# Optimization experiments

Hardware: AMD Instinct MI355X
Metric: run time of the kernel (lower is better)

Reference implementation:

```python
import jax, jax.numpy as jnp
import numpy as np

# SamplesLoss('sinkhorn', p=2, blur=0.05, scaling=0.9), tensorized backend,
# debiased Sinkhorn divergence with log-domain softmin and eps annealing.
P = 2
BLUR = 0.05
SCALING = 0.9
# geomloss uses the data-dependent max diameter; we fix a conservative constant
# (randn clouds in 64-D have pairwise distances ~ sqrt(2*64) ~ 11.3) so the
# epsilon schedule length is static / jit-friendly.
DIAMETER = 16.0


def _eps_schedule():
    e = np.arange(P * np.log(DIAMETER), P * np.log(BLUR), P * np.log(SCALING))
    return np.concatenate([np.exp(e), [BLUR ** P]]).astype(np.float32)  # ~56 steps


def _sqdist(x, y):
    # x: [N,D], y: [M,D] -> [N,M] squared euclidean distances
    return (jnp.sum(x * x, -1)[:, None] + jnp.sum(y * y, -1)[None, :]
            - 2.0 * x @ y.T)


def _softmin(eps, C, h):
    # h: [M] = log-weights + potential/eps ; C: [N,M]
    return -eps * jax.nn.logsumexp(h[None, :] - C / eps, axis=1)


def _sinkhorn_divergence(xb, yb, eps_list):
    # xb: [N,D], yb: [M,D]; uniform weights a=1/N, b=1/M
    N, M = xb.shape[0], yb.shape[0]
    C_xy = 0.5 * _sqdist(xb, yb)   # p=2 cost: |x-y|^2 / 2
    C_yx = C_xy.T
    C_xx = 0.5 * _sqdist(xb, xb)
    C_yy = 0.5 * _sqdist(yb, yb)
    a_log = jnp.full((N,), -float(np.log(N)), C_xy.dtype)
    b_log = jnp.full((M,), -float(np.log(M)), C_xy.dtype)

    # geomloss runs the annealing loop with autograd off; grads come only from
    # the final extrapolation step.
    Cxy_d, Cyx_d, Cxx_d, Cyy_d = map(jax.lax.stop_gradient,
                                     (C_xy, C_yx, C_xx, C_yy))

    eps0 = float(eps_list[0])
    f_ba = _softmin(eps0, Cxy_d, b_log)
    g_ab = _softmin(eps0, Cyx_d, a_log)
    f_aa = _softmin(eps0, Cxx_d, a_log)
    g_bb = _softmin(eps0, Cyy_d, b_log)

    def step(carry, eps):
        f_ba, g_ab, f_aa, g_bb = carry
        ft = _softmin(eps, Cxy_d, b_log + g_ab / eps)
        gt = _softmin(eps, Cyx_d, a_log + f_ba / eps)
        fa = _softmin(eps, Cxx_d, a_log + f_aa / eps)
        gb = _softmin(eps, Cyy_d, b_log + g_bb / eps)
        return (0.5 * (f_ba + ft), 0.5 * (g_ab + gt),
                0.5 * (f_aa + fa), 0.5 * (g_bb + gb)), None

    (f_ba, g_ab, f_aa, g_bb), _ = jax.lax.scan(
        step, (f_ba, g_ab, f_aa, g_bb), jnp.asarray(eps_list))

    # last extrapolation at eps = blur^p, no averaging, with gradients
    eps = float(eps_list[-1])
    f_ba_f = _softmin(eps, C_xy, b_log + g_ab / eps)
    g_ab_f = _softmin(eps, C_yx, a_log + f_ba / eps)
    f_aa_f = _softmin(eps, C_xx, a_log + f_aa / eps)
    g_bb_f = _softmin(eps, C_yy, b_log + g_bb / eps)

    a = jnp.exp(a_log)
    b = jnp.exp(b_log)
    return jnp.dot(a, f_ba_f - f_aa_f) + jnp.dot(b, g_ab_f - g_bb_f)


def setup_inputs() -> dict:
    key = jax.random.key(0)
    k1, k2 = jax.random.split(key)
    x = jax.random.normal(k1, (4, 64, 64, 64), dtype=jnp.float32)
    y = jax.random.normal(k2, (4, 64, 64, 64), dtype=jnp.float32)
    return {"x": x, "y": y}


def reference(x, y):
    B, C, H, W = x.shape
    xf = x.reshape(B, C, H * W).transpose(0, 2, 1)  # [B, N, C]
    yf = y.reshape(B, C, H * W).transpose(0, 2, 1)
    eps_list = _eps_schedule()
    losses = jax.vmap(lambda xb, yb: _sinkhorn_divergence(xb, yb, eps_list))(xf, yf)
    return jnp.sum(losses) / B
```

## Files before the change

kernel.cpp:

```cpp
#include <hip/hip_runtime.h>
#include <cmath>

#define NPTS 4096
#define LOG2E_F 1.4426950408889634f
#define LN2_F   0.6931471805599453f
#define BLOG_F  -8.31776616671934f

#if __has_builtin(__builtin_amdgcn_exp2f)
#define EXP2F(x) __builtin_amdgcn_exp2f(x)
#else
#define EXP2F(x) exp2f(x)
#endif
#if __has_builtin(__builtin_amdgcn_logf)
#define LOG2F(x) __builtin_amdgcn_logf(x)
#else
#define LOG2F(x) log2f(x)
#endif

typedef __attribute__((ext_vector_type(8))) short s16x8;
typedef __attribute__((ext_vector_type(4))) float f32x4;

#define GAS __attribute__((address_space(1)))
#define LAS __attribute__((address_space(3)))

__device__ __forceinline__ ushort bf16h(float f) {
    uint u = __float_as_uint(f);
    return (ushort)((u + 0x7fffu + ((u >> 16) & 1u)) >> 16);
}
__device__ __forceinline__ float bf16tof(ushort h) {
    return __uint_as_float(((uint)h) << 16);
}

__global__ __launch_bounds__(256) void norms_kernel(const float* __restrict__ x,
                                                    const float* __restrict__ y,
                                                    float* __restrict__ norms,
                                                    float* __restrict__ aux0) {
    int flat = blockIdx.x * 256 + threadIdx.x;
    int which = flat >> 14;
    int rem = flat & 16383;
    int b = rem >> 12;
    int i = rem & 4095;
    const float* p = (which ? y : x) + (size_t)b * 64 * NPTS + i;
    float s = 0.f;
#pragma unroll
    for (int c = 0; c < 64; ++c) {
        float v = p[(size_t)c * NPTS];
        s += v * v;
    }
    s *= 0.5f;
    norms[flat] = s;
    aux0[(size_t)((which ? 1 : 0) * 4 + b) * NPTS + i] = -s;
    aux0[(size_t)((which ? 3 : 2) * 4 + b) * NPTS + i] = -s;
}

__global__ __launch_bounds__(256) void split_kernel(const float* __restrict__ x,
                                                    const float* __restrict__ y,
                                                    ushort* __restrict__ split) {
    int flat = blockIdx.x * 256 + threadIdx.x;
    int n = flat & 4095;
    int g = (flat >> 12) & 7;
    int b = (flat >> 15) & 3;
    int which = flat >> 17;
    const float* src = (which ? y : x) + (size_t)b * 64 * NPTS + (size_t)g * 8 * NPTS + n;
    size_t base = ((size_t)(which * 4 + b) * 32 + (n >> 7)) * 2048 + (n & 127);
    ushort hh[8], ll[8];
#pragma unroll
    for (int e = 0; e < 8; ++e) {
        float v = src[(size_t)e * NPTS];
        hh[e] = bf16h(v);
        ll[e] = bf16h(v - bf16tof(hh[e]));
    }
    uint4 hw, lw;
    hw.x = (uint)hh[0] | ((uint)hh[1] << 16);
    hw.y = (uint)hh[2] | ((uint)hh[3] << 16);
    hw.z = (uint)hh[4] | ((uint)hh[5] << 16);
    hw.w = (uint)hh[6] | ((uint)hh[7] << 16);
    lw.x = (uint)ll[0] | ((uint)ll[1] << 16);
    lw.y = (uint)ll[2] | ((uint)ll[3] << 16);
    lw.z = (uint)ll[4] | ((uint)ll[5] << 16);
    lw.w = (uint)ll[6] | ((uint)ll[7] << 16);
    *(uint4*)&split[(base + (size_t)g * 128) * 8]       = hw;
    *(uint4*)&split[(base + (size_t)(g + 8) * 128) * 8] = lw;
}

__global__ __launch_bounds__(256, 4) void softmin_kernel(
    const ushort* __restrict__ split, const float* __restrict__ norms,
    const float* __restrict__ prev, const float* __restrict__ prevaux,
    float* __restrict__ next, float* __restrict__ nextaux,
    float eps, int do_avg)
{
    __shared__ __align__(16) ushort Bt[2][8192];

    const int tid   = threadIdx.x;
    const int bid   = blockIdx.x;
    const int b     = bid & 3;
    const int mat   = (bid >> 2) & 3;
    const int itile = bid >> 4;

    const int row_is_x = (mat == 0 || mat == 2);
    const int col_is_x = (mat == 1 || mat == 2);
    const ushort* rowsplit = split + (size_t)((row_is_x ? 0 : 4) + b) * 32 * 2048 * 8;
    const ushort* colsplit = split + (size_t)((col_is_x ? 0 : 4) + b) * 32 * 2048 * 8;
    const float* rownorm = norms + (row_is_x ? 0 : 16384) + b * NPTS;
    const int hmat = (mat == 0) ? 1 : ((mat == 1) ? 0 : mat);
    const float* hauxv  = prevaux + (size_t)(hmat * 4 + b) * NPTS;
    const float* avgvec = prev + (size_t)(mat  * 4 + b) * NPTS;
    float*       outvec = next + (size_t)(mat  * 4 + b) * NPTS;
    float*       auxvec = nextaux + (size_t)(mat * 4 + b) * NPTS;

    const float se      = (1.0f / eps) * LOG2E_F;
    const float epsblog = eps * BLOG_F;

    const int wave = tid >> 6;
    const int lane = tid & 63;
    const int l16  = lane & 15;
    const int q    = lane >> 4;
    const int i0   = itile * 64;
    const int arow = i0 + wave * 16 + l16;

    s16x8 ah[2], al[2];
    {
        const ushort* abase = rowsplit + ((size_t)(arow >> 7) * 2048 + (arow & 127)) * 8;
#pragma unroll
        for (int kc = 0; kc < 2; ++kc) {
            int g = kc * 4 + q;
            ah[kc] = *(const s16x8*)&abase[(size_t)g * 128 * 8];
            al[kc] = *(const s16x8*)&abase[(size_t)(g + 8) * 128 * 8];
        }
    }

    {
#pragma unroll
        for (int it = 0; it < 4; ++it) {
            int chunk = wave * 256 + it * 64 + lane;
            __builtin_amdgcn_global_load_lds(
                (const GAS uint*)(colsplit + (size_t)chunk * 8),
                (LAS uint*)(&Bt[0][chunk * 8]), 16, 0, 0);
        }
    }
    float hb[8];
#pragma unroll
    for (int t = 0; t < 8; ++t)
        hb[t] = epsblog + hauxv[t * 16 + l16];

    float m[4], l[4];
#pragma unroll
    for (int r = 0; r < 4; ++r) { m[r] = -__builtin_inff(); l[r] = 0.f; }

    __syncthreads();

    for (int jt = 0; jt < 32; ++jt) {
        const int cur = jt & 1;

        float hbn[8];
        if (jt < 31) {
            const ushort* gsrc = colsplit + (size_t)(jt + 1) * 2048 * 8;
#pragma unroll
            for (int it = 0; it < 4; ++it) {
                int chunk = wave * 256 + it * 64 + lane;
                __builtin_amdgcn_global_load_lds(
                    (const GAS uint*)(gsrc + (size_t)chunk * 8),
                    (LAS uint*)(&Bt[cur ^ 1][chunk * 8]), 16, 0, 0);
            }
            const float* hs = hauxv + (jt + 1) * 128;
#pragma unroll
            for (int t = 0; t < 8; ++t)
                hbn[t] = epsblog + hs[t * 16 + l16];
        }

        f32x4 acc[8];
#pragma unroll
        for (int t = 0; t < 8; ++t)
#pragma unroll
            for (int r = 0; r < 4; ++r) acc[t][r] = hb[t];

#pragma unroll
        for (int kc = 0; kc < 2; ++kc) {
            const int gofs = (kc * 4 + q) * 128 * 8;
            s16x8 bf[8];
#pragma unroll
            for (int t = 0; t < 8; ++t)
                bf[t] = *(const s16x8*)&Bt[cur][gofs + (t * 16 + l16) * 8];
#pragma unroll
            for (int t = 0; t < 8; ++t)
                acc[t] = __builtin_amdgcn_mfma_f32_16x16x32_bf16(
                    ah[kc], bf[t], acc[t], 0, 0, 0);
#pragma unroll
            for (int t = 0; t < 8; ++t)
                acc[t] = __builtin_amdgcn_mfma_f32_16x16x32_bf16(
                    al[kc], bf[t], acc[t], 0, 0, 0);
        }

#pragma unroll
        for (int r = 0; r < 4; ++r) {
            float v0 = acc[0][r], v1 = acc[1][r], v2 = acc[2][r], v3 = acc[3][r];
            float v4 = acc[4][r], v5 = acc[5][r], v6 = acc[6][r], v7 = acc[7][r];
            float t0 = fmaxf(fmaxf(v0, v1), fmaxf(v2, v3));
            float t1 = fmaxf(fmaxf(v4, v5), fmaxf(v6, v7));
            float mn = fmaxf(fmaxf(t0, t1), m[r]);
            float tt = -se * mn;
            float e0 = EXP2F(fmaf(v0, se, tt));
            float e1 = EXP2F(fmaf(v1, se, tt));
            float e2 = EXP2F(fmaf(v2, se, tt));
            float e3 = EXP2F(fmaf(v3, se, tt));
            float e4 = EXP2F(fmaf(v4, se, tt));
            float e5 = EXP2F(fmaf(v5, se, tt));
            float e6 = EXP2F(fmaf(v6, se, tt));
            float e7 = EXP2F(fmaf(v7, se, tt));
            float rs = EXP2F(fmaf(m[r], se, tt));
            float sum = ((e0 + e1) + (e2 + e3)) + ((e4 + e5) + (e6 + e7));
            l[r] = fmaf(l[r], rs, sum);
            m[r] = mn;
        }

#pragma unroll
        for (int t = 0; t < 8; ++t) hb[t] = hbn[t];

        __syncthreads();
    }

#pragma unroll
    for (int off = 1; off < 16; off <<= 1) {
#pragma unroll
        for (int r = 0; r < 4; ++r) {
            float mo = __shfl_xor(m[r], off);
            float lo = __shfl_xor(l[r], off);
            float mn = fmaxf(m[r], mo);
            float tt = -se * mn;
            l[r] = fmaf(l[r], EXP2F(fmaf(m[r], se, tt)),
                        lo * EXP2F(fmaf(mo, se, tt)));
            m[r] = mn;
        }
    }

    if (l16 == 0) {
        const float epsln2 = eps * LN2_F;
#pragma unroll
        for (int r = 0; r < 4; ++r) {
            int i = i0 + wave * 16 + q * 4 + r;
            float nrm = rownorm[i];
            float f = nrm - m[r] - epsln2 * LOG2F(l[r]);
            if (do_avg) f = 0.5f * (avgvec[i] + f);
            outvec[i] = f;
            auxvec[i] = f - nrm;
        }
    }
}

__global__ __launch_bounds__(256) void reduce_kernel(const float* __restrict__ fin,
                                                     float* __restrict__ out) {
    float s = 0.f;
    for (int idx = threadIdx.x; idx < 4 * 4 * NPTS; idx += 256) {
        int mat = idx >> 14;
        float v = fin[idx];
        s += (mat < 2) ? v : -v;
    }
#pragma unroll
    for (int off = 32; off > 0; off >>= 1) s += __shfl_down(s, off);
    __shared__ float red[4];
    if ((threadIdx.x & 63) == 0) red[threadIdx.x >> 6] = s;
    __syncthreads();
    if (threadIdx.x == 0) {
        float t = red[0] + red[1] + red[2] + red[3];
        out[0] = t * (1.0f / (4096.0f * 4.0f));
    }
}

extern "C" void kernel_launch(void* const* d_in, const int* in_sizes, int n_in,
                              void* d_out, int out_size, void* d_ws, size_t ws_size,
                              hipStream_t stream) {
    const float* x = (const float*)d_in[0];
    const float* y = (const float*)d_in[1];
    float* out = (float*)d_out;

    float* norms = (float*)d_ws;
    float* bufA  = norms + 32768;
    float* bufB  = bufA + 65536;
    float* auxA  = bufB + 65536;
    float* auxB  = auxA + 65536;
    ushort* split = (ushort*)(auxB + 65536);

    const double start = 2.0 * log(16.0);
    const double stop  = 2.0 * log(0.05);
    const double step  = 2.0 * log(0.9);
    float eps_list[64];
    int ne = 0;
    for (int k = 0;; ++k) {
        double e = start + k * step;
        if (!(e > stop)) break;
        eps_list[ne++] = (float)exp(e);
    }
    eps_list[ne++] = (float)(0.05 * 0.05);

    norms_kernel<<<128, 256, 0, stream>>>(x, y, norms, auxA);
    split_kernel<<<1024, 256, 0, stream>>>(x, y, split);

    softmin_kernel<<<1024, 256, 0, stream>>>(split, norms, bufB, auxA,
                                             bufA, auxB, eps_list[0], 0);
    float* prev = bufA;  float* prevaux = auxB;
    float* next = bufB;  float* nextaux = auxA;
    for (int t = 0; t < ne; ++t) {
        softmin_kernel<<<1024, 256, 0, stream>>>(split, norms, prev, prevaux,
                                                 next, nextaux, eps_list[t], 1);
        float* tf = prev; prev = next; next = tf;
        float* ta = prevaux; prevaux = nextaux; nextaux = ta;
    }
    softmin_kernel<<<1024, 256, 0, stream>>>(split, norms, prev, prevaux,
                                             next, nextaux, eps_list[ne - 1], 0);

    reduce_kernel<<<1, 256, 0, stream>>>(next, out);
}
```

Baseline: 4.833 ms.

## Drop bf16 low-part split, split column range across blocks with merge kernel

Removes the hi/lo bf16 split of the coordinates so the cross term is computed from a single bf16 product, which halves the MFMA work and the staged data. The column dimension is split in two halves across twice as many blocks, each writing partial (max, sum) pairs, and a new merge kernel combines them and applies the averaging. LDS is single-buffered to allow higher occupancy (launch bound 8). This costs precision in the squared-distance cost at small eps, adds an extra launch per iteration, and stages loads without double buffering.

```diff
diff --git a/kernel.cpp b/kernel.cpp
--- a/kernel.cpp
+++ b/kernel.cpp
@@ -26,9 +26,6 @@
 __device__ __forceinline__ ushort bf16h(float f) {
     uint u = __float_as_uint(f);
     return (ushort)((u + 0x7fffu + ((u >> 16) & 1u)) >> 16);
-}
-__device__ __forceinline__ float bf16tof(ushort h) {
-    return __uint_as_float(((uint)h) << 16);
 }
 
 __global__ __launch_bounds__(256) void norms_kernel(const float* __restrict__ x,
@@ -62,51 +59,39 @@
     int b = (flat >> 15) & 3;
     int which = flat >> 17;
     const float* src = (which ? y : x) + (size_t)b * 64 * NPTS + (size_t)g * 8 * NPTS + n;
-    size_t base = ((size_t)(which * 4 + b) * 32 + (n >> 7)) * 2048 + (n & 127);
-    ushort hh[8], ll[8];
-#pragma unroll
-    for (int e = 0; e < 8; ++e) {
-        float v = src[(size_t)e * NPTS];
-        hh[e] = bf16h(v);
-        ll[e] = bf16h(v - bf16tof(hh[e]));
-    }
-    uint4 hw, lw;
+    ushort hh[8];
+#pragma unroll
+    for (int e = 0; e < 8; ++e) hh[e] = bf16h(src[(size_t)e * NPTS]);
+    uint4 hw;
     hw.x = (uint)hh[0] | ((uint)hh[1] << 16);
     hw.y = (uint)hh[2] | ((uint)hh[3] << 16);
     hw.z = (uint)hh[4] | ((uint)hh[5] << 16);
     hw.w = (uint)hh[6] | ((uint)hh[7] << 16);
-    lw.x = (uint)ll[0] | ((uint)ll[1] << 16);
-    lw.y = (uint)ll[2] | ((uint)ll[3] << 16);
-    lw.z = (uint)ll[4] | ((uint)ll[5] << 16);
-    lw.w = (uint)ll[6] | ((uint)ll[7] << 16);
-    *(uint4*)&split[(base + (size_t)g * 128) * 8]       = hw;
-    *(uint4*)&split[(base + (size_t)(g + 8) * 128) * 8] = lw;
-}
-
-__global__ __launch_bounds__(256, 4) void softmin_kernel(
-    const ushort* __restrict__ split, const float* __restrict__ norms,
-    const float* __restrict__ prev, const float* __restrict__ prevaux,
-    float* __restrict__ next, float* __restrict__ nextaux,
-    float eps, int do_avg)
+    size_t dst = ((size_t)(which * 4 + b) * 32 + (n >> 7)) * 8192
+               + (size_t)(g * 128 + (n & 127)) * 8;
+    *(uint4*)&split[dst] = hw;
+}
+
+__global__ __launch_bounds__(256, 8) void softmin_kernel(
+    const ushort* __restrict__ split, const float* __restrict__ prevaux,
+    float2* __restrict__ part, float eps)
 {
-    __shared__ __align__(16) ushort Bt[2][8192];
+    __shared__ __align__(16) ushort Bt[8192];
 
     const int tid   = threadIdx.x;
     const int bid   = blockIdx.x;
     const int b     = bid & 3;
     const int mat   = (bid >> 2) & 3;
-    const int itile = bid >> 4;
+    const int jh    = (bid >> 4) & 1;
+    const int itile = bid >> 5;
 
     const int row_is_x = (mat == 0 || mat == 2);
     const int col_is_x = (mat == 1 || mat == 2);
-    const ushort* rowsplit = split + (size_t)((row_is_x ? 0 : 4) + b) * 32 * 2048 * 8;
-    const ushort* colsplit = split + (size_t)((col_is_x ? 0 : 4) + b) * 32 * 2048 * 8;
-    const float* rownorm = norms + (row_is_x ? 0 : 16384) + b * NPTS;
+    const ushort* rowsplit = split + (size_t)((row_is_x ? 0 : 4) + b) * 32 * 8192;
+    const ushort* colsplit = split + (size_t)((col_is_x ? 0 : 4) + b) * 32 * 8192;
     const int hmat = (mat == 0) ? 1 : ((mat == 1) ? 0 : mat);
-    const float* hauxv  = prevaux + (size_t)(hmat * 4 + b) * NPTS;
-    const float* avgvec = prev + (size_t)(mat  * 4 + b) * NPTS;
-    float*       outvec = next + (size_t)(mat  * 4 + b) * NPTS;
-    float*       auxvec = nextaux + (size_t)(mat * 4 + b) * NPTS;
+    const float* hauxv = prevaux + (size_t)(hmat * 4 + b) * NPTS;
+    float2* partv = part + (size_t)((jh * 4 + mat) * 4 + b) * NPTS;
 
     const float se      = (1.0f / eps) * LOG2E_F;
     const float epsblog = eps * BLOG_F;
@@ -118,50 +103,41 @@
     const int i0   = itile * 64;
     const int arow = i0 + wave * 16 + l16;
 
-    s16x8 ah[2], al[2];
+    s16x8 ah[2];
     {
-        const ushort* abase = rowsplit + ((size_t)(arow >> 7) * 2048 + (arow & 127)) * 8;
-#pragma unroll
-        for (int kc = 0; kc < 2; ++kc) {
-            int g = kc * 4 + q;
-            ah[kc] = *(const s16x8*)&abase[(size_t)g * 128 * 8];
-            al[kc] = *(const s16x8*)&abase[(size_t)(g + 8) * 128 * 8];
-        }
-    }
+        const ushort* abase = rowsplit + (size_t)(arow >> 7) * 8192 + (size_t)(arow & 127) * 8;
+#pragma unroll
+        for (int kc = 0; kc < 2; ++kc)
+            ah[kc] = *(const s16x8*)&abase[(size_t)(kc * 4 + q) * 128 * 8];
+    }
+
+    const int jt0 = jh * 16;
 
     {
+        const ushort* gsrc = colsplit + (size_t)jt0 * 8192;
 #pragma unroll
         for (int it = 0; it < 4; ++it) {
-            int chunk = wave * 256 + it * 64 + lane;
+            int chunk = it * 256 + tid;
             __builtin_amdgcn_global_load_lds(
-                (const GAS uint*)(colsplit + (size_t)chunk * 8),
-                (LAS uint*)(&Bt[0][chunk * 8]), 16, 0, 0);
+                (const GAS uint*)(gsrc + (size_t)chunk * 8),
+                (LAS uint*)(&Bt[chunk * 8]), 16, 0, 0);
         }
     }
     float hb[8];
 #pragma unroll
     for (int t = 0; t < 8; ++t)
-        hb[t] = epsblog + hauxv[t * 16 + l16];
+        hb[t] = epsblog + hauxv[jt0 * 128 + t * 16 + l16];
 
     float m[4], l[4];
 #pragma unroll
     for (int r = 0; r < 4; ++r) { m[r] = -__builtin_inff(); l[r] = 0.f; }
 
-    __syncthreads();
-
-    for (int jt = 0; jt < 32; ++jt) {
-        const int cur = jt & 1;
+    for (int jj = 0; jj < 16; ++jj) {
+        const int jt = jt0 + jj;
+        __syncthreads();
 
         float hbn[8];
-        if (jt < 31) {
-            const ushort* gsrc = colsplit + (size_t)(jt + 1) * 2048 * 8;
-#pragma unroll
-            for (int it = 0; it < 4; ++it) {
-                int chunk = wave * 256 + it * 64 + lane;
-                __builtin_amdgcn_global_load_lds(
-                    (const GAS uint*)(gsrc + (size_t)chunk * 8),
-                    (LAS uint*)(&Bt[cur ^ 1][chunk * 8]), 16, 0, 0);
-            }
+        if (jj < 15) {
             const float* hs = hauxv + (jt + 1) * 128;
 #pragma unroll
             for (int t = 0; t < 8; ++t)
@@ -180,15 +156,24 @@
             s16x8 bf[8];
 #pragma unroll
             for (int t = 0; t < 8; ++t)
-                bf[t] = *(const s16x8*)&Bt[cur][gofs + (t * 16 + l16) * 8];
+                bf[t] = *(const s16x8*)&Bt[gofs + (t * 16 + l16) * 8];
 #pragma unroll
             for (int t = 0; t < 8; ++t)
                 acc[t] = __builtin_amdgcn_mfma_f32_16x16x32_bf16(
                     ah[kc], bf[t], acc[t], 0, 0, 0);
-#pragma unroll
-            for (int t = 0; t < 8; ++t)
-                acc[t] = __builtin_amdgcn_mfma_f32_16x16x32_bf16(
-                    al[kc], bf[t], acc[t], 0, 0, 0);
+        }
+
+        __syncthreads();
+
+        if (jj < 15) {
+            const ushort* gsrc = colsplit + (size_t)(jt + 1) * 8192;
+#pragma unroll
+            for (int it = 0; it < 4; ++it) {
+                int chunk = it * 256 + tid;
+                __builtin_amdgcn_global_load_lds(
+                    (const GAS uint*)(gsrc + (size_t)chunk * 8),
+                    (LAS uint*)(&Bt[chunk * 8]), 16, 0, 0);
+            }
         }
 
 #pragma unroll
@@ -213,10 +198,10 @@
             m[r] = mn;
         }
 
-#pragma unroll
-        for (int t = 0; t < 8; ++t) hb[t] = hbn[t];
-
-        __syncthreads();
+        if (jj < 15) {
+#pragma unroll
+            for (int t = 0; t < 8; ++t) hb[t] = hbn[t];
+        }
     }
 
 #pragma unroll
@@ -234,17 +219,36 @@
     }
 
     if (l16 == 0) {
-        const float epsln2 = eps * LN2_F;
 #pragma unroll
         for (int r = 0; r < 4; ++r) {
-            int i = i0 + wave * 16 + q * 4 + r;
-            float nrm = rownorm[i];
-            float f = nrm - m[r] - epsln2 * LOG2F(l[r]);
-            if (do_avg) f = 0.5f * (avgvec[i] + f);
-            outvec[i] = f;
-            auxvec[i] = f - nrm;
-        }
-    }
+            int row = i0 + wave * 16 + q * 4 + r;
+            partv[row] = make_float2(m[r], l[r]);
+        }
+    }
+}
+
+__global__ __launch_bounds__(256) void merge_kernel(
+    const float2* __restrict__ part, const float* __restrict__ norms,
+    const float* __restrict__ prev, float* __restrict__ next,
+    float* __restrict__ nextaux, float eps, int do_avg)
+{
+    int idx = blockIdx.x * 256 + threadIdx.x;
+    int i = idx & 4095;
+    int b = (idx >> 12) & 3;
+    int mat = idx >> 14;
+    const int row_is_x = (mat == 0 || mat == 2);
+    const float se     = (1.0f / eps) * LOG2E_F;
+    const float epsln2 = eps * LN2_F;
+
+    float nrm = norms[(row_is_x ? 0 : 16384) + b * NPTS + i];
+    float2 p0 = part[(size_t)((0 * 4 + mat) * 4 + b) * NPTS + i];
+    float2 p1 = part[(size_t)((1 * 4 + mat) * 4 + b) * NPTS + i];
+    float mn = fmaxf(p0.x, p1.x);
+    float lc = p0.y * EXP2F((p0.x - mn) * se) + p1.y * EXP2F((p1.x - mn) * se);
+    float f = nrm - mn - epsln2 * LOG2F(lc);
+    if (do_avg) f = 0.5f * (prev[idx] + f);
+    next[idx] = f;
+    nextaux[idx] = f - nrm;
 }
 
 __global__ __launch_bounds__(256) void reduce_kernel(const float* __restrict__ fin,
@@ -278,7 +282,8 @@
     float* bufB  = bufA + 65536;
     float* auxA  = bufB + 65536;
     float* auxB  = auxA + 65536;
-    ushort* split = (ushort*)(auxB + 65536);
+    float2* part = (float2*)(auxB + 65536);
+    ushort* split = (ushort*)(part + 131072);
 
     const double start = 2.0 * log(16.0);
     const double stop  = 2.0 * log(0.05);
@@ -295,18 +300,21 @@
     norms_kernel<<<128, 256, 0, stream>>>(x, y, norms, auxA);
     split_kernel<<<1024, 256, 0, stream>>>(x, y, split);
 
-    softmin_kernel<<<1024, 256, 0, stream>>>(split, norms, bufB, auxA,
-                                             bufA, auxB, eps_list[0], 0);
+    softmin_kernel<<<2048, 256, 0, stream>>>(split, auxA, part, eps_list[0]);
+    merge_kernel<<<256, 256, 0, stream>>>(part, norms, bufB, bufA, auxB,
+                                          eps_list[0], 0);
     float* prev = bufA;  float* prevaux = auxB;
     float* next = bufB;  float* nextaux = auxA;
     for (int t = 0; t < ne; ++t) {
-        softmin_kernel<<<1024, 256, 0, stream>>>(split, norms, prev, prevaux,
-                                                 next, nextaux, eps_list[t], 1);
+        softmin_kernel<<<2048, 256, 0, stream>>>(split, prevaux, part, eps_list[t]);
+        merge_kernel<<<256, 256, 0, stream>>>(part, norms, prev, next, nextaux,
+                                              eps_list[t], 1);
         float* tf = prev; prev = next; next = tf;
         float* ta = prevaux; prevaux = nextaux; nextaux = ta;
     }
-    softmin_kernel<<<1024, 256, 0, stream>>>(split, norms, prev, prevaux,
-                                             next, nextaux, eps_list[ne - 1], 0);
+    softmin_kernel<<<2048, 256, 0, stream>>>(split, prevaux, part, eps_list[ne - 1]);
+    merge_kernel<<<256, 256, 0, stream>>>(part, norms, prev, next, nextaux,
+                                          eps_list[ne - 1], 0);
 
     reduce_kernel<<<1, 256, 0, stream>>>(next, out);
 }
```

After: 6.535 ms. 1.35x slower.
